# Kernel tuning notes

Hardware: AMD Instinct MI355X
Metric: run time of the kernel (lower is better)

## Reference

```python
import jax, jax.numpy as jnp
import numpy as np

N = 20000        # num_nodes
E = 320000       # num_edges
B = 2            # batch_size (query rows)
F = 64           # in_features == nrela_dim == out_features
R = 32           # num_relations
NEG_SLOPE = 0.2  # LeakyReLU alpha
RATIO = 0.5      # fixed ratio (ratio-given branch of forward)
ITERS = 4
LN_EPS = 1e-5


def setup_inputs() -> dict:
    key = jax.random.key(0)
    ks = jax.random.split(key, 12)
    return {
        "edge_index": jax.random.randint(ks[0], (2, E), 0, N),
        "r_index": jax.random.randint(ks[1], (E,), 0, R),
        "boudnary_input": jax.random.normal(ks[2], (N, B, F), dtype=jnp.float32),
        "query_input": jax.random.normal(ks[3], (B, F), dtype=jnp.float32),
        # relation_linear: in_features -> nrela_dim * num_relations (torch [out,in] layout)
        "rel_w": 0.02 * jax.random.normal(ks[4], (R * F, F), dtype=jnp.float32),
        "rel_b": jnp.zeros((R * F,), dtype=jnp.float32),
        # layer_linear: 2*in_features -> out_features
        "layer_w": 0.02 * jax.random.normal(ks[5], (F, 2 * F), dtype=jnp.float32),
        "layer_b": jnp.zeros((F,), dtype=jnp.float32),
        # trans_readout_linear: in_features -> out_features
        "tr_w": 0.02 * jax.random.normal(ks[6], (F, F), dtype=jnp.float32),
        "tr_b": jnp.zeros((F,), dtype=jnp.float32),
        "W": 0.02 * jax.random.normal(ks[7], (B * F, F), dtype=jnp.float32),
        "a": 0.02 * jax.random.normal(ks[8], (4, F, 1), dtype=jnp.float32),
        "ln_g": jnp.ones((F,), dtype=jnp.float32),
        "ln_b": jnp.zeros((F,), dtype=jnp.float32),
    }


def _one_iter(x, i, edge_index, r_index, query, rel_w, rel_b, layer_w, layer_b,
              tr_w, tr_b, W, a, ln_g, ln_b):
    src, dst = edge_index[0], edge_index[1]
    node_in = x[src]                                           # [E, B, F] gather
    rel = (query @ rel_w.T + rel_b).reshape(R, B, F)           # [R, B, F]
    edge_in = rel[r_index]                                     # [E, B, F]
    msg = node_in + edge_in                                    # [E, B, F]
    edge_h = msg.reshape(E, B * F) @ W                         # [E, F]
    alpha = jax.nn.leaky_relu(jnp.squeeze(edge_h @ a[i], -1), NEG_SLOPE)  # [E]
    # sparse softmax grouped by source node
    m = jax.ops.segment_max(alpha, src, num_segments=N)
    ex = jnp.exp(alpha - m[src])
    denom = jax.ops.segment_sum(ex, src, num_segments=N)
    alpha = ex / (denom[src] + 1e-16)
    # top-k mask over all edges
    k = int(E * RATIO)
    _, idx = jax.lax.top_k(alpha, k)
    mask = jnp.zeros((E,), dtype=bool).at[idx].set(True)
    alpha = jnp.where(mask, alpha, 0.0)
    # path_message: scatter-add of weighted messages by dst; the concatenated
    # self-loop part (ones * boundary scattered by arange) is exactly + x
    update = jax.ops.segment_sum(alpha[:, None, None] * msg, dst, num_segments=N) + x
    readout = jnp.mean(x, axis=0)                              # [B, F]
    out = jnp.concatenate([x, update], axis=-1) @ layer_w.T + layer_b  # [N, B, F]
    out = out + (readout @ tr_w.T + tr_b)                      # broadcast [B, F]
    mu = out.mean(-1, keepdims=True)
    var = out.var(-1, keepdims=True)
    out = (out - mu) / jnp.sqrt(var + LN_EPS) * ln_g + ln_b
    return jax.nn.elu(out)


def reference(edge_index, r_index, boudnary_input, query_input, rel_w, rel_b,
              layer_w, layer_b, tr_w, tr_b, W, a, ln_g, ln_b):
    x = boudnary_input
    for i in range(ITERS):  # ratio-given branch: iter_layer = 0..3
        h = _one_iter(x, i, edge_index, r_index, query_input, rel_w, rel_b,
                      layer_w, layer_b, tr_w, tr_b, W, a, ln_g, ln_b)
        x = h + x
    return x
```

## Files before the change

### kernel.cpp

```cpp
#include <hip/hip_runtime.h>
#include <stdint.h>

#define NN 20000
#define EE 320000
#define FF 64
#define ROW 128
#define KTOP 160000
#define NEG_SLOPE 0.2f
#define LN_EPS 1e-5f
#define H16BINS 16384
#define HBASE (120 << 11)
#define CCAP 16384

__device__ __forceinline__ unsigned int bin_of(unsigned int u) {
  int b = (int)(u >> 12) - HBASE;
  b = b < 0 ? 0 : (b > (H16BINS - 1) ? (H16BINS - 1) : b);
  return (unsigned int)b;
}

__global__ void precompute_kernel(const float* __restrict__ query,
                                  const float* __restrict__ rel_w,
                                  const float* __restrict__ rel_b,
                                  const float* __restrict__ W,
                                  const float* __restrict__ a,
                                  float* __restrict__ relflat,
                                  float* __restrict__ wa4) {
  int t = blockIdx.x * blockDim.x + threadIdx.x;
  if (t < 4096) {
    int bq = t >> 11, c = t & 2047;
    const float* q = query + bq * FF;
    const float* w = rel_w + (size_t)c * FF;
    float s = rel_b[c];
#pragma unroll
    for (int f = 0; f < FF; f++) s += q[f] * w[f];
    relflat[t] = s;
  }
  if (t < 512) {
    int i = t >> 7, j = t & 127;
    const float* av = a + i * FF;
    const float* w = W + (size_t)j * FF;
    float s = 0.f;
#pragma unroll
    for (int f = 0; f < FF; f++) s += w[f] * av[f];
    wa4[t] = s;
  }
}

__global__ void degcnt_kernel(const int* __restrict__ esrc, const int* __restrict__ edst,
                              unsigned int* __restrict__ deg_s, unsigned int* __restrict__ deg_d) {
  int e = blockIdx.x * blockDim.x + threadIdx.x;
  if (e < EE) {
    atomicAdd(deg_s + esrc[e], 1u);
    atomicAdd(deg_d + edst[e], 1u);
  }
}

__global__ void scan_kernel(const unsigned int* __restrict__ deg,
                            unsigned int* __restrict__ rowptr,
                            unsigned int* __restrict__ rowfill) {
  __shared__ unsigned int sh[1024];
  int t = threadIdx.x;
  const int PER = 20;
  unsigned int loc[PER];
  unsigned int sum = 0;
  int base = t * PER;
#pragma unroll
  for (int i = 0; i < PER; i++) {
    int n = base + i;
    unsigned int d = (n < NN) ? deg[n] : 0u;
    loc[i] = sum;
    sum += d;
  }
  sh[t] = sum;
  __syncthreads();
  for (int o = 1; o < 1024; o <<= 1) {
    unsigned int v = (t >= o) ? sh[t - o] : 0u;
    __syncthreads();
    sh[t] += v;
    __syncthreads();
  }
  unsigned int excl = sh[t] - sum;
#pragma unroll
  for (int i = 0; i < PER; i++) {
    int n = base + i;
    if (n < NN) {
      unsigned int rp = excl + loc[i];
      rowptr[n] = rp;
      rowfill[n] = rp;
    }
  }
  if (t == 1023) rowptr[NN] = EE;
}

__global__ void fill_kernel(const int* __restrict__ esrc, const int* __restrict__ edst,
                            const int* __restrict__ rix,
                            unsigned int* __restrict__ rowfill_s, unsigned int* __restrict__ rowfill_d,
                            unsigned int* __restrict__ cspack_s, int* __restrict__ csre_d) {
  int e = blockIdx.x * blockDim.x + threadIdx.x;
  if (e < EE) {
    unsigned int r = (unsigned int)rix[e];
    unsigned int ss = atomicAdd(rowfill_s + esrc[e], 1u);
    cspack_s[ss] = (unsigned int)e | (r << 19);
    unsigned int sd = atomicAdd(rowfill_d + edst[e], 1u);
    csre_d[sd] = e;
  }
}

__global__ void gatherd_kernel(const int* __restrict__ csre_d, const int* __restrict__ esrc,
                               const int* __restrict__ rix, unsigned int* __restrict__ packed_d,
                               unsigned int* __restrict__ pos_d) {
  int p = blockIdx.x * blockDim.x + threadIdx.x;
  if (p < EE) {
    int e = csre_d[p];
    packed_d[p] = (unsigned int)esrc[e] | ((unsigned int)rix[e] << 20);
    pos_d[e] = (unsigned int)p;
  }
}

__global__ void repack_kernel(unsigned int* __restrict__ cspack_s,
                              const unsigned int* __restrict__ pos_d) {
  int i = blockIdx.x * blockDim.x + threadIdx.x;
  if (i < EE) {
    unsigned int cs = cspack_s[i];
    cspack_s[i] = pos_d[cs & 0x7FFFFu] | (cs & 0xFFF80000u);
  }
}

__global__ void readout_kernel(const float* __restrict__ x, float* __restrict__ racc) {
  int j = threadIdx.x;
  float acc = 0.f;
  for (int n = blockIdx.x; n < NN; n += gridDim.x) acc += x[(size_t)n * ROW + j];
  atomicAdd(racc + j, acc);
}

__global__ void nodewa_kernel(const float* __restrict__ x, const float* __restrict__ wa,
                              float* __restrict__ nodewa) {
  int wave = threadIdx.x >> 6, lane = threadIdx.x & 63;
  float w0 = wa[lane], w1 = wa[64 + lane];
  for (int n = blockIdx.x * 4 + wave; n < NN; n += gridDim.x * 4) {
    float s = x[(size_t)n * ROW + lane] * w0 + x[(size_t)n * ROW + 64 + lane] * w1;
#pragma unroll
    for (int off = 32; off > 0; off >>= 1) s += __shfl_xor(s, off, 64);
    if (lane == 0) nodewa[n] = s;
  }
}

__global__ __launch_bounds__(256) void alpha_csr_kernel(
    const unsigned int* __restrict__ rowptr_s, const unsigned int* __restrict__ cspack_s,
    const float* __restrict__ nodewa, const float* __restrict__ relflat,
    const float* __restrict__ wa, float* __restrict__ alpha_d,
    unsigned int* __restrict__ hist16, unsigned int* __restrict__ state) {
  __shared__ float relwa_sh[32];
  __shared__ unsigned int h16[H16BINS];
  int t = threadIdx.x;
  for (int i = t; i < H16BINS; i += 256) h16[i] = 0u;
  if (t < 32) {
    float s = 0.f;
    const float4* rf = (const float4*)(relflat + t * ROW);
    const float4* wf = (const float4*)wa;
#pragma unroll 8
    for (int j = 0; j < 32; j++) {
      float4 r4 = rf[j], w4 = wf[j];
      s += r4.x * w4.x + r4.y * w4.y + r4.z * w4.z + r4.w * w4.w;
    }
    relwa_sh[t] = s;
  }
  if (blockIdx.x == 0 && t == 255) { state[0] = 0u; state[1] = KTOP; }
  __syncthreads();
  int n = blockIdx.x * 256 + t;
  if (n < NN) {
    unsigned int p0 = rowptr_s[n], p1 = rowptr_s[n + 1];
    float nw = nodewa[n];
    float denom = 0.f;
    for (unsigned int p = p0; p < p1; p++) {
      unsigned int cs = cspack_s[p];
      float v = nw + relwa_sh[cs >> 19];
      v = v > 0.f ? v : NEG_SLOPE * v;
      denom += expf(v);
    }
    float inv = 1.0f / denom;
    for (unsigned int p = p0; p < p1; p++) {
      unsigned int cs = cspack_s[p];
      float v = nw + relwa_sh[cs >> 19];
      v = v > 0.f ? v : NEG_SLOPE * v;
      float av = expf(v) * inv;
      alpha_d[cs & 0x7FFFFu] = av;
      atomicAdd(&h16[bin_of(__float_as_uint(av))], 1u);
    }
  }
  __syncthreads();
  for (int i = t; i < H16BINS; i += 256) {
    unsigned int c = h16[i];
    if (c) atomicAdd(hist16 + i, c);
  }
}

__global__ void sel16_kernel(unsigned int* __restrict__ state, const unsigned int* __restrict__ hist16) {
  __shared__ unsigned int sh[1024];
  int t = threadIdx.x;
  unsigned int s = 0;
  const unsigned int* hp = hist16 + t * (H16BINS / 1024);
#pragma unroll
  for (int i = 0; i < H16BINS / 1024; i++) s += hp[i];
  sh[t] = s;
  __syncthreads();
  for (int o = 1; o < 1024; o <<= 1) {
    unsigned int v = (t >= o) ? sh[t - o] : 0u;
    __syncthreads();
    sh[t] += v;
    __syncthreads();
  }
  unsigned int incl = sh[t];
  unsigned int total = sh[1023];
  unsigned int krem = state[1];
  unsigned int cumAbove = total - incl;
  if (t == 0) state[5] = 0u;
  if (cumAbove < krem && cumAbove + s >= krem) {
    unsigned int cum = cumAbove;
    for (int b = H16BINS / 1024 - 1; b >= 0; b--) {
      unsigned int c = hist16[t * (H16BINS / 1024) + b];
      if (cum + c >= krem) {
        state[0] = (unsigned int)(t * (H16BINS / 1024) + b);
        state[1] = krem - cum;
        break;
      }
      cum += c;
    }
  }
}

__global__ void cand_kernel(const float* __restrict__ alpha_d, unsigned int* __restrict__ state,
                            int* __restrict__ cand_p) {
  __shared__ int lbuf[256];
  __shared__ unsigned int lcnt;
  __shared__ unsigned int gbase;
  int t = threadIdx.x;
  if (t == 0) lcnt = 0u;
  __syncthreads();
  int p = blockIdx.x * 256 + t;
  if (p < EE) {
    unsigned int u = __float_as_uint(alpha_d[p]);
    if (bin_of(u) == state[0]) {
      unsigned int idx = atomicAdd(&lcnt, 1u);
      lbuf[idx] = p;
    }
  }
  __syncthreads();
  if (t == 0 && lcnt) gbase = atomicAdd(state + 5, lcnt);
  __syncthreads();
  if (t < (int)lcnt) {
    unsigned int pos = gbase + t;
    if (pos < CCAP) cand_p[pos] = lbuf[t];
  }
}

__global__ void final_kernel(float* __restrict__ alpha_d, const int* __restrict__ csre_d,
                             const int* __restrict__ cand_p, unsigned int* __restrict__ state) {
  __shared__ unsigned int hlow[4096];
  __shared__ unsigned int psum[256];
  __shared__ int tiebuf[2048];
  __shared__ unsigned int tcnt;
  __shared__ unsigned int sT, sNeed;
  int t = threadIdx.x;
  unsigned int cnt = state[5];
  if (cnt > CCAP) cnt = CCAP;
  unsigned int krem = state[1];
  for (int i = t; i < 4096; i += 256) hlow[i] = 0u;
  if (t == 0) { tcnt = 0u; sT = 0u; sNeed = 0xFFFFFFFFu; }
  __syncthreads();
  for (unsigned int i = t; i < cnt; i += 256)
    atomicAdd(&hlow[__float_as_uint(alpha_d[cand_p[i]]) & 0xFFFu], 1u);
  __syncthreads();
  unsigned int s = 0;
#pragma unroll
  for (int i = 0; i < 16; i++) s += hlow[t * 16 + i];
  psum[t] = s;
  __syncthreads();
  for (int o = 1; o < 256; o <<= 1) {
    unsigned int v = (t >= o) ? psum[t - o] : 0u;
    __syncthreads();
    psum[t] += v;
    __syncthreads();
  }
  unsigned int total = psum[255];
  unsigned int above_chunk = total - psum[t];
  if (above_chunk < krem && above_chunk + s >= krem) {
    unsigned int cum = above_chunk;
    for (int b = 15; b >= 0; b--) {
      unsigned int c = hlow[t * 16 + b];
      if (cum + c >= krem) {
        sT = ((state[0] + (unsigned int)HBASE) << 12) | (unsigned int)(t * 16 + b);
        sNeed = krem - cum;
        break;
      }
      cum += c;
    }
  }
  __syncthreads();
  unsigned int T = sT, need = sNeed;
  if (t == 0) { state[2] = T; state[3] = need; }
  for (unsigned int i = t; i < cnt; i += 256) {
    int p = cand_p[i];
    if (__float_as_uint(alpha_d[p]) == T) {
      unsigned int idx = atomicAdd(&tcnt, 1u);
      if (idx < 2048) tiebuf[idx] = p;
    }
  }
  __syncthreads();
  unsigned int tc = tcnt;
  if (tc > 2048) tc = 2048;
  if (tc > need) {
    for (unsigned int i = t; i < tc; i += 256) {
      int p = tiebuf[i];
      int e_i = csre_d[p];
      unsigned int rank = 0;
      for (unsigned int j = 0; j < tc; j++) rank += (csre_d[tiebuf[j]] < e_i) ? 1u : 0u;
      if (rank >= need) alpha_d[p] = 0.f;
    }
  }
}

__global__ __launch_bounds__(256) void update_kernel(const unsigned int* __restrict__ rowptr_d,
                                                     const unsigned int* __restrict__ packed_d,
                                                     const float* __restrict__ alpha_d,
                                                     const unsigned int* __restrict__ state,
                                                     const float* __restrict__ x,
                                                     const float* __restrict__ relflat,
                                                     float* __restrict__ upd,
                                                     float* __restrict__ racc_next) {
  __shared__ float relf[32 * 132];
  int t = threadIdx.x;
  if (blockIdx.x == 0 && t < 128) racc_next[t] = 0.f;
#pragma unroll
  for (int i = 0; i < 4; i++) {
    int q = t + i * 256;
    int r = q >> 5, kq = q & 31;
    float4 v = ((const float4*)relflat)[q];
    *(float4*)(relf + r * 132 + kq * 4) = v;
  }
  __syncthreads();
  unsigned int T = state[2];
  int wave = t >> 6, lane = t & 63;
  int g = lane >> 4, l = lane & 15;
  int n = blockIdx.x * 4 + wave;
  if (n >= NN) return;
  unsigned int p0 = rowptr_d[n], p1 = rowptr_d[n + 1];
  float4 A0 = {0.f, 0.f, 0.f, 0.f}, A1 = {0.f, 0.f, 0.f, 0.f};
  for (unsigned int base = p0 + g; base < p1; base += 4) {
    float w = alpha_d[base];
    if (__float_as_uint(w) < T) continue;
    unsigned int up = packed_d[base];
    unsigned int src = up & 0xFFFFFu;
    unsigned int r = up >> 20;
    const float* xr = x + (size_t)src * ROW + l * 8;
    const float* rr = relf + r * 132 + l * 8;
    float4 xv0 = *(const float4*)xr;
    float4 xv1 = *(const float4*)(xr + 4);
    float4 rv0 = *(const float4*)rr;
    float4 rv1 = *(const float4*)(rr + 4);
    A0.x += w * (xv0.x + rv0.x); A0.y += w * (xv0.y + rv0.y);
    A0.z += w * (xv0.z + rv0.z); A0.w += w * (xv0.w + rv0.w);
    A1.x += w * (xv1.x + rv1.x); A1.y += w * (xv1.y + rv1.y);
    A1.z += w * (xv1.z + rv1.z); A1.w += w * (xv1.w + rv1.w);
  }
#pragma unroll
  for (int off = 16; off <= 32; off <<= 1) {
    A0.x += __shfl_xor(A0.x, off, 64); A0.y += __shfl_xor(A0.y, off, 64);
    A0.z += __shfl_xor(A0.z, off, 64); A0.w += __shfl_xor(A0.w, off, 64);
    A1.x += __shfl_xor(A1.x, off, 64); A1.y += __shfl_xor(A1.y, off, 64);
    A1.z += __shfl_xor(A1.z, off, 64); A1.w += __shfl_xor(A1.w, off, 64);
  }
  if (g == 0) {
    const float* xn = x + (size_t)n * ROW + l * 8;
    float4 xs0 = *(const float4*)xn;
    float4 xs1 = *(const float4*)(xn + 4);
    float4 o0 = {A0.x + xs0.x, A0.y + xs0.y, A0.z + xs0.z, A0.w + xs0.w};
    float4 o1 = {A1.x + xs1.x, A1.y + xs1.y, A1.z + xs1.z, A1.w + xs1.w};
    float* on = upd + (size_t)n * ROW + l * 8;
    *(float4*)on = o0;
    *(float4*)(on + 4) = o1;
  }
}

__global__ __launch_bounds__(256) void node_gemm_kernel(const float* __restrict__ upd,
                                                        const float* __restrict__ layer_w,
                                                        const float* __restrict__ layer_b,
                                                        const float* __restrict__ racc_cur,
                                                        const float* __restrict__ tr_w,
                                                        const float* __restrict__ tr_b,
                                                        const float* __restrict__ ln_g,
                                                        const float* __restrict__ ln_b,
                                                        float* __restrict__ x,
                                                        const float* __restrict__ wa_next,
                                                        float* __restrict__ nodewa,
                                                        float* __restrict__ racc_next) {
  __shared__ float As[64 * 132];
  __shared__ float Ws[64 * 132];
  __shared__ float trt_sh[128];
  __shared__ float racc_sh[128];
  __shared__ float nodewa_sh[32];
  int t = threadIdx.x;
  int n0 = blockIdx.x * 32;
  if (t < 128) {
    int b = t >> 6, f = t & 63;
    const float invN = 1.0f / (float)NN;
    float s = tr_b[f] + layer_b[f];
    const float* rr = racc_cur + b * 64;
    const float* tw = tr_w + f * 64;
#pragma unroll 16
    for (int gg = 0; gg < 64; gg++) s += rr[gg] * invN * tw[gg];
    trt_sh[t] = s;
    racc_sh[t] = 0.f;
  }
  if (t < 32) nodewa_sh[t] = 0.f;
#pragma unroll
  for (int i = 0; i < 4; i++) {
    int v = t + i * 256;
    int nl = v >> 5, i4 = v & 31;
    int b = i4 >> 4, kq = i4 & 15;
    int m = nl * 2 + b;
    float4 xv = ((const float4*)x)[n0 * 32 + v];
    *(float4*)(As + m * 132 + kq * 4) = xv;
  }
#pragma unroll
  for (int i = 0; i < 4; i++) {
    int v = t + i * 256;
    int nl = v >> 5, i4 = v & 31;
    int b = i4 >> 4, kq = i4 & 15;
    int m = nl * 2 + b;
    float4 uv = ((const float4*)upd)[n0 * 32 + v];
    *(float4*)(As + m * 132 + 64 + kq * 4) = uv;
  }
#pragma unroll
  for (int i = 0; i < 8; i++) {
    int Q = t + i * 256;
    int f = Q >> 5, q = Q & 31;
    float4 wv = ((const float4*)layer_w)[Q];
    *(float4*)(Ws + f * 132 + ((q ^ ((f >> 2) & 7)) << 2)) = wv;
  }
  __syncthreads();
  int tx = t & 15, ty = t >> 4;
  float acc[4][4] = {};
  const float* Abase = As + (ty * 4) * 132;
  const float* Wbase = Ws + (tx * 4) * 132;
  int wswz = tx & 7;
#pragma unroll 4
  for (int kq = 0; kq < 32; kq++) {
    float4 a0 = *(const float4*)(Abase + 0 * 132 + kq * 4);
    float4 a1 = *(const float4*)(Abase + 1 * 132 + kq * 4);
    float4 a2 = *(const float4*)(Abase + 2 * 132 + kq * 4);
    float4 a3 = *(const float4*)(Abase + 3 * 132 + kq * 4);
    int wq = (kq ^ wswz) << 2;
    float4 w0 = *(const float4*)(Wbase + 0 * 132 + wq);
    float4 w1 = *(const float4*)(Wbase + 1 * 132 + wq);
    float4 w2 = *(const float4*)(Wbase + 2 * 132 + wq);
    float4 w3 = *(const float4*)(Wbase + 3 * 132 + wq);
#define DOT4(A, W) (A.x * W.x + A.y * W.y + A.z * W.z + A.w * W.w)
    acc[0][0] += DOT4(a0, w0); acc[0][1] += DOT4(a0, w1); acc[0][2] += DOT4(a0, w2); acc[0][3] += DOT4(a0, w3);
    acc[1][0] += DOT4(a1, w0); acc[1][1] += DOT4(a1, w1); acc[1][2] += DOT4(a1, w2); acc[1][3] += DOT4(a1, w3);
    acc[2][0] += DOT4(a2, w0); acc[2][1] += DOT4(a2, w1); acc[2][2] += DOT4(a2, w2); acc[2][3] += DOT4(a2, w3);
    acc[3][0] += DOT4(a3, w0); acc[3][1] += DOT4(a3, w1); acc[3][2] += DOT4(a3, w2); acc[3][3] += DOT4(a3, w3);
#undef DOT4
  }
#pragma unroll
  for (int r = 0; r < 4; r++) {
    const float* tp = trt_sh + ((r & 1) << 6) + tx * 4;
#pragma unroll
    for (int c = 0; c < 4; c++) acc[r][c] += tp[c];
  }
  float s[4], qq[4];
#pragma unroll
  for (int r = 0; r < 4; r++) {
    s[r] = acc[r][0] + acc[r][1] + acc[r][2] + acc[r][3];
    qq[r] = acc[r][0] * acc[r][0] + acc[r][1] * acc[r][1] + acc[r][2] * acc[r][2] + acc[r][3] * acc[r][3];
  }
#pragma unroll
  for (int off = 1; off < 16; off <<= 1) {
#pragma unroll
    for (int r = 0; r < 4; r++) {
      s[r] += __shfl_xor(s[r], off, 64);
      qq[r] += __shfl_xor(qq[r], off, 64);
    }
  }
  float4 g4 = ((const float4*)ln_g)[tx];
  float4 b4 = ((const float4*)ln_b)[tx];
  float4 wn = ((const float4*)wa_next)[tx];
  float4 wn1 = ((const float4*)wa_next)[16 + tx];
  const float invF = 1.0f / (float)FF;
  float nwc[2] = {0.f, 0.f};
#pragma unroll
  for (int r = 0; r < 4; r++) {
    float mu = s[r] * invF;
    float var = qq[r] * invF - mu * mu;
    float rstd = 1.0f / sqrtf(var + LN_EPS);
    int m = ty * 4 + r;
    int nl = m >> 1, b = m & 1;
    float4 xo = ((const float4*)x)[(n0 + nl) * 32 + b * 16 + tx];
    float o0 = (acc[r][0] - mu) * rstd * g4.x + b4.x;
    float o1 = (acc[r][1] - mu) * rstd * g4.y + b4.y;
    float o2 = (acc[r][2] - mu) * rstd * g4.z + b4.z;
    float o3 = (acc[r][3] - mu) * rstd * g4.w + b4.w;
    float4 y;
    y.x = (o0 > 0.f ? o0 : expm1f(o0)) + xo.x;
    y.y = (o1 > 0.f ? o1 : expm1f(o1)) + xo.y;
    y.z = (o2 > 0.f ? o2 : expm1f(o2)) + xo.z;
    y.w = (o3 > 0.f ? o3 : expm1f(o3)) + xo.w;
    ((float4*)x)[(n0 + nl) * 32 + b * 16 + tx] = y;
    float* rs = racc_sh + (b << 6) + tx * 4;
    atomicAdd(rs + 0, y.x); atomicAdd(rs + 1, y.y);
    atomicAdd(rs + 2, y.z); atomicAdd(rs + 3, y.w);
    float4 w = b ? wn1 : wn;
    nwc[r >> 1] += y.x * w.x + y.y * w.y + y.z * w.z + y.w * w.w;
  }
  atomicAdd(&nodewa_sh[ty * 2 + 0], nwc[0]);
  atomicAdd(&nodewa_sh[ty * 2 + 1], nwc[1]);
  __syncthreads();
  if (t < 128) atomicAdd(racc_next + t, racc_sh[t]);
  if (t < 32) nodewa[n0 + t] = nodewa_sh[t];
}

extern "C" void kernel_launch(void* const* d_in, const int* in_sizes, int n_in,
                              void* d_out, int out_size, void* d_ws, size_t ws_size,
                              hipStream_t stream) {
  const int* ei = (const int*)d_in[0];
  const int* esrc = ei;
  const int* edst = ei + EE;
  const int* rix = (const int*)d_in[1];
  const float* boundary = (const float*)d_in[2];
  const float* query = (const float*)d_in[3];
  const float* rel_w = (const float*)d_in[4];
  const float* rel_b = (const float*)d_in[5];
  const float* layer_w = (const float*)d_in[6];
  const float* layer_b = (const float*)d_in[7];
  const float* tr_w = (const float*)d_in[8];
  const float* tr_b = (const float*)d_in[9];
  const float* Wm = (const float*)d_in[10];
  const float* av = (const float*)d_in[11];
  const float* ln_g = (const float*)d_in[12];
  const float* ln_b = (const float*)d_in[13];
  float* x = (float*)d_out;

  char* ws = (char*)d_ws;
  size_t off = 0;
  auto allocf = [&](size_t n) -> float* {
    float* p = (float*)(ws + off);
    off += ((n * 4 + 255) / 256) * 256;
    return p;
  };
  auto allocu = [&](size_t n) -> unsigned int* {
    unsigned int* p = (unsigned int*)(ws + off);
    off += ((n * 4 + 255) / 256) * 256;
    return p;
  };
  float* relflat = allocf(4096);
  float* wa4 = allocf(512);
  float* alpha_d = allocf(EE);
  float* upd = allocf((size_t)NN * ROW);
  float* racc0 = allocf(128);
  float* racc1 = allocf(128);
  float* nodewa = allocf(NN);
  unsigned int* hist16 = allocu(H16BINS);
  unsigned int* state = allocu(8);
  unsigned int* deg_s = allocu(NN);
  unsigned int* deg_d = allocu(NN);
  unsigned int* rowptr_s = allocu(NN + 1);
  unsigned int* rowptr_d = allocu(NN + 1);
  unsigned int* rowfill_s = allocu(NN);
  unsigned int* rowfill_d = allocu(NN);
  unsigned int* cspack_s = allocu(EE);
  int* csre_d = (int*)allocu(EE);
  unsigned int* packed_d = allocu(EE);
  unsigned int* pos_d = allocu(EE);
  int* cand_p = (int*)allocu(CCAP);
  float* rbuf[2] = {racc0, racc1};

  hipMemcpyAsync(x, boundary, (size_t)NN * ROW * 4, hipMemcpyDeviceToDevice, stream);
  hipMemsetAsync(deg_s, 0, NN * 4, stream);
  hipMemsetAsync(deg_d, 0, NN * 4, stream);
  hipMemsetAsync(racc0, 0, 128 * 4, stream);
  precompute_kernel<<<16, 256, 0, stream>>>(query, rel_w, rel_b, Wm, av, relflat, wa4);

  degcnt_kernel<<<EE / 256, 256, 0, stream>>>(esrc, edst, deg_s, deg_d);
  scan_kernel<<<1, 1024, 0, stream>>>(deg_s, rowptr_s, rowfill_s);
  scan_kernel<<<1, 1024, 0, stream>>>(deg_d, rowptr_d, rowfill_d);
  fill_kernel<<<EE / 256, 256, 0, stream>>>(esrc, edst, rix, rowfill_s, rowfill_d, cspack_s, csre_d);
  gatherd_kernel<<<EE / 256, 256, 0, stream>>>(csre_d, esrc, rix, packed_d, pos_d);
  repack_kernel<<<EE / 256, 256, 0, stream>>>(cspack_s, pos_d);

  readout_kernel<<<256, 128, 0, stream>>>(x, racc0);
  nodewa_kernel<<<1250, 256, 0, stream>>>(x, wa4, nodewa);

  for (int it = 0; it < 4; it++) {
    float* rcur = rbuf[it & 1];
    float* rnxt = rbuf[(it + 1) & 1];
    const float* wa_it = wa4 + it * 128;
    const float* wa_nx = wa4 + (it < 3 ? it + 1 : 3) * 128;

    hipMemsetAsync(hist16, 0, H16BINS * 4, stream);
    alpha_csr_kernel<<<(NN + 255) / 256, 256, 0, stream>>>(rowptr_s, cspack_s, nodewa,
                                                           relflat, wa_it, alpha_d, hist16, state);
    sel16_kernel<<<1, 1024, 0, stream>>>(state, hist16);
    cand_kernel<<<EE / 256, 256, 0, stream>>>(alpha_d, state, cand_p);
    final_kernel<<<1, 256, 0, stream>>>(alpha_d, csre_d, cand_p, state);

    update_kernel<<<5000, 256, 0, stream>>>(rowptr_d, packed_d, alpha_d, state, x, relflat,
                                            upd, rnxt);
    node_gemm_kernel<<<625, 256, 0, stream>>>(upd, layer_w, layer_b, rcur, tr_w, tr_b,
                                              ln_g, ln_b, x, wa_nx, nodewa, rnxt);
  }
}
```

Baseline: 738.3 us.

## Use bf16 MFMA for node GEMM and move readout transform to separate kernel

Replaces the FP32 FMA-tiled node GEMM with bf16 MFMA 16x16x32 instructions, staging inputs and weights as bf16 in LDS and rewriting the LayerNorm/ELU epilogue for the MFMA output layout. The readout transform computation is moved out of each of the 625 blocks into a tiny per-iteration kernel. Histogram zeroing moves from a memset into the selection kernel. This lowers GEMM compute cost and per-block redundant work, but adds bf16 rounding error to the node update and an extra launch per iteration.

```diff
diff --git a/kernel.cpp b/kernel.cpp
--- a/kernel.cpp
+++ b/kernel.cpp
@@ -11,11 +11,28 @@
 #define H16BINS 16384
 #define HBASE (120 << 11)
 #define CCAP 16384
+#define ASTR 136
+
+typedef __attribute__((ext_vector_type(8))) short short8;
+typedef __attribute__((ext_vector_type(4))) float f32x4;
 
 __device__ __forceinline__ unsigned int bin_of(unsigned int u) {
   int b = (int)(u >> 12) - HBASE;
   b = b < 0 ? 0 : (b > (H16BINS - 1) ? (H16BINS - 1) : b);
   return (unsigned int)b;
+}
+
+__device__ __forceinline__ unsigned int f2bf(float v) {
+  unsigned int u = __float_as_uint(v);
+  return (u + 0x7FFFu + ((u >> 16) & 1u)) >> 16;
+}
+
+__device__ __forceinline__ unsigned long long pack4bf(float4 v) {
+  unsigned long long a = (unsigned long long)f2bf(v.x);
+  a |= (unsigned long long)f2bf(v.y) << 16;
+  a |= (unsigned long long)f2bf(v.z) << 32;
+  a |= (unsigned long long)f2bf(v.w) << 48;
+  return a;
 }
 
 __global__ void precompute_kernel(const float* __restrict__ query,
@@ -145,6 +162,20 @@
   }
 }
 
+__global__ void trt_kernel(const float* __restrict__ racc_cur, const float* __restrict__ tr_w,
+                           const float* __restrict__ tr_b, const float* __restrict__ layer_b,
+                           float* __restrict__ trt_glob) {
+  int t = threadIdx.x;
+  int b = t >> 6, f = t & 63;
+  const float invN = 1.0f / (float)NN;
+  float s = tr_b[f] + layer_b[f];
+  const float* rr = racc_cur + b * 64;
+  const float* tw = tr_w + f * 64;
+#pragma unroll 16
+  for (int g = 0; g < 64; g++) s += rr[g] * invN * tw[g];
+  trt_glob[t] = s;
+}
+
 __global__ __launch_bounds__(256) void alpha_csr_kernel(
     const unsigned int* __restrict__ rowptr_s, const unsigned int* __restrict__ cspack_s,
     const float* __restrict__ nodewa, const float* __restrict__ relflat,
@@ -195,7 +226,7 @@
   }
 }
 
-__global__ void sel16_kernel(unsigned int* __restrict__ state, const unsigned int* __restrict__ hist16) {
+__global__ void sel16_kernel(unsigned int* __restrict__ state, unsigned int* __restrict__ hist16) {
   __shared__ unsigned int sh[1024];
   int t = threadIdx.x;
   unsigned int s = 0;
@@ -227,6 +258,7 @@
       cum += c;
     }
   }
+  for (int i = 0; i < H16BINS / 1024; i++) hist16[t * (H16BINS / 1024) + i] = 0u;
 }
 
 __global__ void cand_kernel(const float* __restrict__ alpha_d, unsigned int* __restrict__ state,
@@ -382,141 +414,113 @@
   }
 }
 
-__global__ __launch_bounds__(256) void node_gemm_kernel(const float* __restrict__ upd,
+__global__ __launch_bounds__(256) void node_mfma_kernel(const float* __restrict__ upd,
                                                         const float* __restrict__ layer_w,
-                                                        const float* __restrict__ layer_b,
-                                                        const float* __restrict__ racc_cur,
-                                                        const float* __restrict__ tr_w,
-                                                        const float* __restrict__ tr_b,
+                                                        const float* __restrict__ trt_glob,
                                                         const float* __restrict__ ln_g,
                                                         const float* __restrict__ ln_b,
                                                         float* __restrict__ x,
                                                         const float* __restrict__ wa_next,
                                                         float* __restrict__ nodewa,
                                                         float* __restrict__ racc_next) {
-  __shared__ float As[64 * 132];
-  __shared__ float Ws[64 * 132];
+  __shared__ unsigned short Asb[64 * ASTR];
+  __shared__ unsigned short Wsb[64 * ASTR];
   __shared__ float trt_sh[128];
   __shared__ float racc_sh[128];
-  __shared__ float nodewa_sh[32];
   int t = threadIdx.x;
   int n0 = blockIdx.x * 32;
-  if (t < 128) {
-    int b = t >> 6, f = t & 63;
-    const float invN = 1.0f / (float)NN;
-    float s = tr_b[f] + layer_b[f];
-    const float* rr = racc_cur + b * 64;
-    const float* tw = tr_w + f * 64;
-#pragma unroll 16
-    for (int gg = 0; gg < 64; gg++) s += rr[gg] * invN * tw[gg];
-    trt_sh[t] = s;
-    racc_sh[t] = 0.f;
-  }
-  if (t < 32) nodewa_sh[t] = 0.f;
+  if (t < 128) { trt_sh[t] = trt_glob[t]; racc_sh[t] = 0.f; }
 #pragma unroll
   for (int i = 0; i < 4; i++) {
     int v = t + i * 256;
-    int nl = v >> 5, i4 = v & 31;
-    int b = i4 >> 4, kq = i4 & 15;
-    int m = nl * 2 + b;
+    int m = ((v >> 5) << 1) + ((v & 31) >> 4);
+    int k = (v & 15) * 4;
     float4 xv = ((const float4*)x)[n0 * 32 + v];
-    *(float4*)(As + m * 132 + kq * 4) = xv;
-  }
-#pragma unroll
-  for (int i = 0; i < 4; i++) {
-    int v = t + i * 256;
-    int nl = v >> 5, i4 = v & 31;
-    int b = i4 >> 4, kq = i4 & 15;
-    int m = nl * 2 + b;
+    *(unsigned long long*)(Asb + m * ASTR + k) = pack4bf(xv);
     float4 uv = ((const float4*)upd)[n0 * 32 + v];
-    *(float4*)(As + m * 132 + 64 + kq * 4) = uv;
+    *(unsigned long long*)(Asb + m * ASTR + 64 + k) = pack4bf(uv);
   }
 #pragma unroll
   for (int i = 0; i < 8; i++) {
     int Q = t + i * 256;
-    int f = Q >> 5, q = Q & 31;
+    int f = Q >> 5, c4 = Q & 31;
     float4 wv = ((const float4*)layer_w)[Q];
-    *(float4*)(Ws + f * 132 + ((q ^ ((f >> 2) & 7)) << 2)) = wv;
-  }
-  __syncthreads();
-  int tx = t & 15, ty = t >> 4;
-  float acc[4][4] = {};
-  const float* Abase = As + (ty * 4) * 132;
-  const float* Wbase = Ws + (tx * 4) * 132;
-  int wswz = tx & 7;
-#pragma unroll 4
-  for (int kq = 0; kq < 32; kq++) {
-    float4 a0 = *(const float4*)(Abase + 0 * 132 + kq * 4);
-    float4 a1 = *(const float4*)(Abase + 1 * 132 + kq * 4);
-    float4 a2 = *(const float4*)(Abase + 2 * 132 + kq * 4);
-    float4 a3 = *(const float4*)(Abase + 3 * 132 + kq * 4);
-    int wq = (kq ^ wswz) << 2;
-    float4 w0 = *(const float4*)(Wbase + 0 * 132 + wq);
-    float4 w1 = *(const float4*)(Wbase + 1 * 132 + wq);
-    float4 w2 = *(const float4*)(Wbase + 2 * 132 + wq);
-    float4 w3 = *(const float4*)(Wbase + 3 * 132 + wq);
-#define DOT4(A, W) (A.x * W.x + A.y * W.y + A.z * W.z + A.w * W.w)
-    acc[0][0] += DOT4(a0, w0); acc[0][1] += DOT4(a0, w1); acc[0][2] += DOT4(a0, w2); acc[0][3] += DOT4(a0, w3);
-    acc[1][0] += DOT4(a1, w0); acc[1][1] += DOT4(a1, w1); acc[1][2] += DOT4(a1, w2); acc[1][3] += DOT4(a1, w3);
-    acc[2][0] += DOT4(a2, w0); acc[2][1] += DOT4(a2, w1); acc[2][2] += DOT4(a2, w2); acc[2][3] += DOT4(a2, w3);
-    acc[3][0] += DOT4(a3, w0); acc[3][1] += DOT4(a3, w1); acc[3][2] += DOT4(a3, w2); acc[3][3] += DOT4(a3, w3);
-#undef DOT4
-  }
+    *(unsigned long long*)(Wsb + f * ASTR + c4 * 4) = pack4bf(wv);
+  }
+  __syncthreads();
+  int lane = t & 63, mt = t >> 6;
+  int l15 = lane & 15, q = lane >> 4;
+  const unsigned short* arow = Asb + (mt * 16 + l15) * ASTR + q * 8;
+  f32x4 acc[4] = {{0.f, 0.f, 0.f, 0.f}, {0.f, 0.f, 0.f, 0.f},
+                  {0.f, 0.f, 0.f, 0.f}, {0.f, 0.f, 0.f, 0.f}};
+#pragma unroll
+  for (int ks = 0; ks < 4; ks++) {
+    short8 a = *(const short8*)(arow + ks * 32);
+#pragma unroll
+    for (int nt = 0; nt < 4; nt++) {
+      short8 b = *(const short8*)(Wsb + (nt * 16 + l15) * ASTR + ks * 32 + q * 8);
+      acc[nt] = __builtin_amdgcn_mfma_f32_16x16x32_bf16(a, b, acc[nt], 0, 0, 0);
+    }
+  }
+  float g_[4], bta[4], wn0[4], wn1[4], tr0[4], tr1[4];
+#pragma unroll
+  for (int nt = 0; nt < 4; nt++) {
+    int f = nt * 16 + l15;
+    g_[nt] = ln_g[f]; bta[nt] = ln_b[f];
+    wn0[nt] = wa_next[f]; wn1[nt] = wa_next[64 + f];
+    tr0[nt] = trt_sh[f]; tr1[nt] = trt_sh[64 + f];
+  }
+  const float invF = 1.0f / (float)FF;
+  float y[4][4];
 #pragma unroll
   for (int r = 0; r < 4; r++) {
-    const float* tp = trt_sh + ((r & 1) << 6) + tx * 4;
-#pragma unroll
-    for (int c = 0; c < 4; c++) acc[r][c] += tp[c];
-  }
-  float s[4], qq[4];
-#pragma unroll
-  for (int r = 0; r < 4; r++) {
-    s[r] = acc[r][0] + acc[r][1] + acc[r][2] + acc[r][3];
-    qq[r] = acc[r][0] * acc[r][0] + acc[r][1] * acc[r][1] + acc[r][2] * acc[r][2] + acc[r][3] * acc[r][3];
-  }
-#pragma unroll
-  for (int off = 1; off < 16; off <<= 1) {
-#pragma unroll
-    for (int r = 0; r < 4; r++) {
-      s[r] += __shfl_xor(s[r], off, 64);
-      qq[r] += __shfl_xor(qq[r], off, 64);
-    }
-  }
-  float4 g4 = ((const float4*)ln_g)[tx];
-  float4 b4 = ((const float4*)ln_b)[tx];
-  float4 wn = ((const float4*)wa_next)[tx];
-  float4 wn1 = ((const float4*)wa_next)[16 + tx];
-  const float invF = 1.0f / (float)FF;
-  float nwc[2] = {0.f, 0.f};
-#pragma unroll
-  for (int r = 0; r < 4; r++) {
-    float mu = s[r] * invF;
-    float var = qq[r] * invF - mu * mu;
+    int b = r & 1;
+    float o[4];
+    float s = 0.f, qq = 0.f;
+#pragma unroll
+    for (int nt = 0; nt < 4; nt++) {
+      float v = acc[nt][r] + (b ? tr1[nt] : tr0[nt]);
+      o[nt] = v; s += v; qq += v * v;
+    }
+#pragma unroll
+    for (int off = 1; off < 16; off <<= 1) {
+      s += __shfl_xor(s, off, 64);
+      qq += __shfl_xor(qq, off, 64);
+    }
+    float mu = s * invF;
+    float var = qq * invF - mu * mu;
     float rstd = 1.0f / sqrtf(var + LN_EPS);
-    int m = ty * 4 + r;
-    int nl = m >> 1, b = m & 1;
-    float4 xo = ((const float4*)x)[(n0 + nl) * 32 + b * 16 + tx];
-    float o0 = (acc[r][0] - mu) * rstd * g4.x + b4.x;
-    float o1 = (acc[r][1] - mu) * rstd * g4.y + b4.y;
-    float o2 = (acc[r][2] - mu) * rstd * g4.z + b4.z;
-    float o3 = (acc[r][3] - mu) * rstd * g4.w + b4.w;
-    float4 y;
-    y.x = (o0 > 0.f ? o0 : expm1f(o0)) + xo.x;
-    y.y = (o1 > 0.f ? o1 : expm1f(o1)) + xo.y;
-    y.z = (o2 > 0.f ? o2 : expm1f(o2)) + xo.z;
-    y.w = (o3 > 0.f ? o3 : expm1f(o3)) + xo.w;
-    ((float4*)x)[(n0 + nl) * 32 + b * 16 + tx] = y;
-    float* rs = racc_sh + (b << 6) + tx * 4;
-    atomicAdd(rs + 0, y.x); atomicAdd(rs + 1, y.y);
-    atomicAdd(rs + 2, y.z); atomicAdd(rs + 3, y.w);
-    float4 w = b ? wn1 : wn;
-    nwc[r >> 1] += y.x * w.x + y.y * w.y + y.z * w.z + y.w * w.w;
-  }
-  atomicAdd(&nodewa_sh[ty * 2 + 0], nwc[0]);
-  atomicAdd(&nodewa_sh[ty * 2 + 1], nwc[1]);
+    int nl = mt * 8 + q * 2 + (r >> 1);
+    size_t base = (size_t)(n0 + nl) * ROW + b * 64 + l15;
+#pragma unroll
+    for (int nt = 0; nt < 4; nt++) {
+      float xo = x[base + nt * 16];
+      float on = (o[nt] - mu) * rstd * g_[nt] + bta[nt];
+      float h = on > 0.f ? on : expm1f(on);
+      float yy = h + xo;
+      y[r][nt] = yy;
+      x[base + nt * 16] = yy;
+    }
+  }
+#pragma unroll
+  for (int b = 0; b < 2; b++) {
+#pragma unroll
+    for (int nt = 0; nt < 4; nt++) {
+      atomicAdd(&racc_sh[b * 64 + nt * 16 + l15], y[b][nt] + y[b + 2][nt]);
+    }
+  }
+#pragma unroll
+  for (int rp = 0; rp < 2; rp++) {
+    float nw = 0.f;
+#pragma unroll
+    for (int nt = 0; nt < 4; nt++)
+      nw += y[2 * rp][nt] * wn0[nt] + y[2 * rp + 1][nt] * wn1[nt];
+#pragma unroll
+    for (int off = 1; off < 16; off <<= 1) nw += __shfl_xor(nw, off, 64);
+    if (l15 == 0) nodewa[n0 + mt * 8 + q * 2 + rp] = nw;
+  }
   __syncthreads();
   if (t < 128) atomicAdd(racc_next + t, racc_sh[t]);
-  if (t < 32) nodewa[n0 + t] = nodewa_sh[t];
 }
 
 extern "C" void kernel_launch(void* const* d_in, const int* in_sizes, int n_in,
@@ -558,6 +562,7 @@
   float* upd = allocf((size_t)NN * ROW);
   float* racc0 = allocf(128);
   float* racc1 = allocf(128);
+  float* trt_glob = allocf(128);
   float* nodewa = allocf(NN);
   unsigned int* hist16 = allocu(H16BINS);
   unsigned int* state = allocu(8);
@@ -578,6 +583,7 @@
   hipMemsetAsync(deg_s, 0, NN * 4, stream);
   hipMemsetAsync(deg_d, 0, NN * 4, stream);
   hipMemsetAsync(racc0, 0, 128 * 4, stream);
+  hipMemsetAsync(hist16, 0, H16BINS * 4, stream);
   precompute_kernel<<<16, 256, 0, stream>>>(query, rel_w, rel_b, Wm, av, relflat, wa4);
 
   degcnt_kernel<<<EE / 256, 256, 0, stream>>>(esrc, edst, deg_s, deg_d);
@@ -596,7 +602,7 @@
     const float* wa_it = wa4 + it * 128;
     const float* wa_nx = wa4 + (it < 3 ? it + 1 : 3) * 128;
 
-    hipMemsetAsync(hist16, 0, H16BINS * 4, stream);
+    trt_kernel<<<1, 128, 0, stream>>>(rcur, tr_w, tr_b, layer_b, trt_glob);
     alpha_csr_kernel<<<(NN + 255) / 256, 256, 0, stream>>>(rowptr_s, cspack_s, nodewa,
                                                            relflat, wa_it, alpha_d, hist16, state);
     sel16_kernel<<<1, 1024, 0, stream>>>(state, hist16);
@@ -605,7 +611,7 @@
 
     update_kernel<<<5000, 256, 0, stream>>>(rowptr_d, packed_d, alpha_d, state, x, relflat,
                                             upd, rnxt);
-    node_gemm_kernel<<<625, 256, 0, stream>>>(upd, layer_w, layer_b, rcur, tr_w, tr_b,
-                                              ln_g, ln_b, x, wa_nx, nodewa, rnxt);
-  }
-}
+    node_mfma_kernel<<<625, 256, 0, stream>>>(upd, layer_w, trt_glob, ln_g, ln_b, x,
+                                              wa_nx, nodewa, rnxt);
+  }
+}
```

Measured after the change: 694.9 us. 1.06x faster.
